# Optimization experiments

Hardware: AMD Instinct MI355X
Metric: run time of the kernel (lower is better)

Reference implementation:

```python
import jax, jax.numpy as jnp
import numpy as np

EPS = 1e-5
HEADS = 8  # heads kwarg of TransformerDecoder


def _ln(x, g, b):
    mu = jnp.mean(x, axis=-1, keepdims=True)
    var = jnp.var(x, axis=-1, keepdims=True)
    return (x - mu) * jax.lax.rsqrt(var + EPS) * g + b


def _expert(params, xt, m, scale):
    """One TransformerDecoder expert (BIT-style): per layer, PreNorm2 cross-attn + residual,
    then PreNorm FeedForward + residual. xt: (B,S,D), m: (B,Nt,D)."""
    an_g, an_b, wq, wk, wv, wo, wo_b, fn_g, fn_b, w1, b1, w2, b2 = params
    L = an_g.shape[0]
    B, S, D = xt.shape
    Nt = m.shape[1]
    for l in range(L):
        xn = _ln(xt, an_g[l], an_b[l])
        mn = _ln(m, an_g[l], an_b[l])  # PreNorm2 norms both streams with the same LN
        q = (xn @ wq[l]).reshape(B, S, HEADS, -1)
        k = (mn @ wk[l]).reshape(B, Nt, HEADS, -1)
        v = (mn @ wv[l]).reshape(B, Nt, HEADS, -1)
        attn = jax.nn.softmax(jnp.einsum('bihd,bjhd->bhij', q, k) * scale, axis=-1)
        o = jnp.einsum('bhij,bjhd->bihd', attn, v).reshape(B, S, -1)
        xt = xt + o @ wo[l] + wo_b[l]
        h = _ln(xt, fn_g[l], fn_b[l])
        xt = xt + jax.nn.gelu(h @ w1[l] + b1[l], approximate=False) @ w2[l] + b2[l]
    return xt


def setup_inputs():
    key = jax.random.key(0)
    ks = iter(jax.random.split(key, 40))
    B, C, H, W = 4, 128, 64, 64
    D, INNER, FF, P, L, NT = 256, 512, 1024, 4, 2, 8
    r = lambda shape, s=1.0: jax.random.normal(next(ks), shape, jnp.float32) * s
    return {
        'x': r((B, C, H, W)),
        'm': r((B, NT, D)),
        'proj_w': r((C, D), 0.05), 'proj_b': r((D,), 0.02),
        'lnp_g': jnp.ones((D,), jnp.float32), 'lnp_b': jnp.zeros((D,), jnp.float32),
        'sq_w': r((D, D), 0.05), 'sq_b': r((D,), 0.02),
        'sk_w': r((D, D), 0.05), 'sk_b': r((D,), 0.02),
        'sv_w': r((D, 1), 0.05), 'sv_b': r((1,), 0.02),
        'an_g': jnp.ones((P, L, D), jnp.float32), 'an_b': jnp.zeros((P, L, D), jnp.float32),
        'wq': r((P, L, D, INNER), 0.05), 'wk': r((P, L, D, INNER), 0.05), 'wv': r((P, L, D, INNER), 0.05),
        'wo': r((P, L, INNER, D), 0.05), 'wo_b': r((P, L, D), 0.02),
        'fn_g': jnp.ones((P, L, D), jnp.float32), 'fn_b': jnp.zeros((P, L, D), jnp.float32),
        'w1': r((P, L, D, FF), 0.05), 'b1': r((P, L, FF), 0.02),
        'w2': r((P, L, FF, D), 0.05), 'b2': r((P, L, D), 0.02),
        'fln_g': jnp.ones((D,), jnp.float32), 'fln_b': jnp.zeros((D,), jnp.float32),
    }


def reference(x, m, proj_w, proj_b, lnp_g, lnp_b, sq_w, sq_b, sk_w, sk_b, sv_w, sv_b,
              an_g, an_b, wq, wk, wv, wo, wo_b, fn_g, fn_b, w1, b1, w2, b2, fln_g, fln_b):
    B, C, H, W = x.shape
    D = proj_w.shape[1]
    # 1x1 conv -> flatten(2).transpose(1,2): row-major (h,w) tokens
    tokens = jnp.einsum('bchw,cd->bhwd', x, proj_w).reshape(B, H * W, D) + proj_b
    tokens = _ln(tokens, lnp_g, lnp_b)
    # TokenScorer: cross-attention importance scores, v projects to scalar
    q = tokens @ sq_w + sq_b
    k = m @ sk_w + sk_b
    v = m @ sv_w + sv_b  # (B, Nt, 1)
    aw = jax.nn.softmax(jnp.einsum('bnd,bmd->bnm', q, k) / jnp.sqrt(jnp.float32(D)), axis=-1)
    scores = jnp.einsum('bnm,bmo->bno', aw, v)[..., 0]  # (B, N)
    P = an_g.shape[0]
    N = tokens.shape[1]
    S = N // P
    # descending sort of token scores
    idx = jnp.argsort(-scores, axis=1)  # (B, N)
    pscores = jnp.take_along_axis(scores, idx, axis=1).reshape(B, P, S).mean(-1)  # (B, P)
    pw = jax.nn.softmax(pscores, axis=1)  # (B, P)
    # gather tokens per partition: (P, B, S, D)
    gathered = jnp.take_along_axis(tokens, idx[..., None], axis=1).reshape(B, P, S, D).transpose(1, 0, 2, 3)
    scale = 1.0 / jnp.sqrt(jnp.float32(D))  # Cross_Attention scale = dim ** -0.5
    params = (an_g, an_b, wq, wk, wv, wo, wo_b, fn_g, fn_b, w1, b1, w2, b2)
    proc = jax.vmap(lambda pr, xt: _expert(pr, xt, m, scale))(params, gathered)  # (P, B, S, D)
    proc = proc * pw.T[:, :, None, None]
    flat = proc.transpose(1, 0, 2, 3).reshape(B, N, D)
    # scatter back into original token order (idx is a permutation)
    out = jnp.zeros_like(tokens).at[jnp.arange(B)[:, None], idx].set(flat)
    return _ln(out, fln_g, fln_b)
```

## Files before the change

kernel.cpp:

```cpp
#include <hip/hip_runtime.h>
#include <hip/hip_bf16.h>
#include <math.h>

#define BB 4
#define CC 128
#define NN 4096
#define DD 256
#define INNER 512
#define FFD 1024
#define PP 4
#define LL 2
#define NT 8
#define SS 1024
#define SCALE 0.0625f

typedef __attribute__((ext_vector_type(8))) short bf16x8;
typedef __attribute__((ext_vector_type(8))) short short8;
typedef __attribute__((ext_vector_type(4))) short short4v;
typedef __attribute__((ext_vector_type(4))) float f32x4;

#define GLD_LDS16(g, l) __builtin_amdgcn_global_load_lds( \
    (const __attribute__((address_space(1))) void*)(g), \
    (__attribute__((address_space(3))) void*)(l), 16, 0, 0)

template<int NW>
__device__ inline float block_sum(float v, float* sbuf){
  #pragma unroll
  for (int mk=32; mk; mk>>=1) v += __shfl_xor(v, mk);
  int w = threadIdx.x>>6;
  if ((threadIdx.x&63)==0) sbuf[w]=v;
  __syncthreads();
  float r = 0.f;
  #pragma unroll
  for (int k=0;k<NW;k++) r += sbuf[k];
  __syncthreads();
  return r;
}

__device__ inline unsigned short bf16bits(float v){
  __hip_bfloat16 t = __float2bfloat16(v);
  unsigned short u;
  __builtin_memcpy(&u, &t, 2);
  return u;
}
__device__ inline float bf2f(unsigned short u){
  unsigned int x = ((unsigned int)u)<<16;
  float f;
  __builtin_memcpy(&f, &x, 4);
  return f;
}

__device__ inline float gelu_f(float x){
  float z  = x * 0.70710678118654752440f;
  float az = fabsf(z);
  float t  = 1.0f / (1.0f + 0.3275911f*az);
  float y  = t*(0.254829592f + t*(-0.284496736f + t*(1.421413741f +
             t*(-1.453152027f + t*1.061405429f))));
  float erfv = 1.0f - y*__expf(-az*az);
  erfv = (z < 0.0f) ? -erfv : erfv;
  return 0.5f*x*(1.0f+erfv);
}

__global__ __launch_bounds__(256) void scorer_kernel(
    const float* __restrict__ m, const float* __restrict__ sk_w,
    const float* __restrict__ sk_b, const float* __restrict__ sv_w,
    const float* __restrict__ sv_b, const float* __restrict__ sq_w,
    const float* __restrict__ sq_b,
    float* __restrict__ kk2, float* __restrict__ kb, float* __restrict__ vsc)
{
  __shared__ float ms[256];
  __shared__ float ks[256];
  __shared__ float sbuf[4];
  int bj = blockIdx.x;
  int tid = threadIdx.x;
  ms[tid] = m[bj*DD + tid];
  __syncthreads();
  float acc=0.f;
  #pragma unroll 8
  for(int c=0;c<DD;c++) acc = fmaf(ms[c], sk_w[c*DD + tid], acc);
  ks[tid] = acc + sk_b[tid];
  float sv = block_sum<4>(ms[tid]*sv_w[tid], sbuf);
  if(tid==0) vsc[bj] = sv + sv_b[0];
  __syncthreads();
  const float* wr = sq_w + (long)tid*DD;
  float a2 = 0.f;
  #pragma unroll 4
  for (int c=0; c<DD; c+=4){
    float4 wvv = *(const float4*)(wr + c);
    a2 = fmaf(wvv.x, ks[c+0], fmaf(wvv.y, ks[c+1], fmaf(wvv.z, ks[c+2], fmaf(wvv.w, ks[c+3], a2))));
  }
  kk2[bj*DD + tid] = a2;
  float kbv = block_sum<4>(sq_b[tid]*ks[tid], sbuf);
  if (tid==0) kb[bj] = kbv;
}

__global__ __launch_bounds__(256) void proj_prep_kernel(
    const float* __restrict__ x, const float* __restrict__ proj_w,
    const float* __restrict__ proj_b, const float* __restrict__ lnp_g,
    const float* __restrict__ lnp_b, const float* __restrict__ kk2,
    const float* __restrict__ kb, const float* __restrict__ vsc,
    float* __restrict__ tokens, float* __restrict__ scores,
    int* __restrict__ rank, long long* __restrict__ psumsI,
    const float* __restrict__ m, const float* __restrict__ an_g,
    const float* __restrict__ an_b, const float* __restrict__ wk,
    const float* __restrict__ wv, float* __restrict__ kvk,
    float* __restrict__ kvv,
    const float* __restrict__ wq, const float* __restrict__ w1,
    const float* __restrict__ w2,
    __hip_bfloat16* __restrict__ wqT, __hip_bfloat16* __restrict__ w1T,
    __hip_bfloat16* __restrict__ w2T)
{
  __shared__ union {
    struct {
      float xs[16][132];
      float ys[16][260];
      float kj[8][260];
      float kbs[8], vs[8], mu_s[16], rs_s[16];
      float lg[16][8];
    } pr;
    struct { float t[64][65]; } wc;
    struct { float mn[256]; float sbuf[4]; } kv;
  } sm;
  int z = blockIdx.x;
  int tid = threadIdx.x;

  if (z < 1024){
    int b  = z >> 8;
    int n0 = (z & 255) * 16;
    if (tid < 16) rank[b*NN + n0 + tid] = 0;
    if (z == 0 && tid < 16) psumsI[tid] = 0;
    float (*xs)[132] = sm.pr.xs;
    float (*ys)[260] = sm.pr.ys;
    float (*kj)[260] = sm.pr.kj;
    float* kbs = sm.pr.kbs; float* vs = sm.pr.vs;
    float* mu_s = sm.pr.mu_s; float* rs_s = sm.pr.rs_s;
    float (*lg)[8] = sm.pr.lg;
    #pragma unroll
    for (int i=0;i<8;i++){
      int l = tid + i*256;
      int t = l & 15, c = l >> 4;
      xs[t][c] = x[(long)(b*CC + c)*NN + n0 + t];
    }
    #pragma unroll
    for (int i=0;i<8;i++){
      int idx = i*256 + tid;
      int r = idx >> 8, c = idx & 255;
      kj[r][c] = kk2[(b*NT + r)*DD + c];
    }
    if (tid < 8){ kbs[tid] = kb[b*NT+tid]; vs[tid] = vsc[b*NT+tid]; }
    __syncthreads();
    float acc[16];
    #pragma unroll
    for (int t=0;t<16;t++) acc[t]=0.f;
    for (int c0=0;c0<CC;c0+=4){
      float w0 = proj_w[(c0+0)*DD + tid];
      float w1_ = proj_w[(c0+1)*DD + tid];
      float w2_ = proj_w[(c0+2)*DD + tid];
      float w3_ = proj_w[(c0+3)*DD + tid];
      #pragma unroll
      for (int t=0;t<16;t++){
        float4 xv = *(const float4*)&xs[t][c0];
        acc[t] = fmaf(xv.x,w0,fmaf(xv.y,w1_,fmaf(xv.z,w2_,fmaf(xv.w,w3_,acc[t]))));
      }
    }
    float pb = proj_b[tid];
    #pragma unroll
    for (int t=0;t<16;t++) ys[t][tid] = acc[t] + pb;
    __syncthreads();
    int w = tid>>6, lane = tid&63;
    for (int k=0;k<4;k++){
      int t = w*4+k;
      float s = ys[t][lane] + ys[t][lane+64] + ys[t][lane+128] + ys[t][lane+192];
      #pragma unroll
      for (int mk=32; mk; mk>>=1) s += __shfl_xor(s, mk);
      float mu = s*(1.0f/256.0f);
      float d0=ys[t][lane]-mu, d1=ys[t][lane+64]-mu, d2=ys[t][lane+128]-mu, d3=ys[t][lane+192]-mu;
      float q = d0*d0+d1*d1+d2*d2+d3*d3;
      #pragma unroll
      for (int mk=32; mk; mk>>=1) q += __shfl_xor(q, mk);
      if (lane==0){ mu_s[t]=mu; rs_s[t]=rsqrtf(q*(1.0f/256.0f)+1e-5f); }
    }
    __syncthreads();
    float g = lnp_g[tid], be = lnp_b[tid];
    #pragma unroll
    for (int t=0;t<16;t++){
      float nv = (ys[t][tid]-mu_s[t])*rs_s[t]*g + be;
      tokens[((long)(b*NN + n0 + t))*DD + tid] = nv;
      ys[t][tid] = nv;
    }
    __syncthreads();
    if (tid < 128){
      int t = tid>>3, j = tid&7;
      float a2 = 0.f;
      for (int c0=0;c0<DD;c0+=4){
        float4 tv = *(const float4*)&ys[t][c0];
        float4 kv2 = *(const float4*)&kj[j][c0];
        a2 = fmaf(tv.x,kv2.x,fmaf(tv.y,kv2.y,fmaf(tv.z,kv2.z,fmaf(tv.w,kv2.w,a2))));
      }
      lg[t][j] = (a2 + kbs[j]) * SCALE;
    }
    __syncthreads();
    if (tid < 16){
      float mx=-1e30f;
      #pragma unroll
      for(int j=0;j<NT;j++) mx=fmaxf(mx,lg[tid][j]);
      float s=0.f, sc=0.f;
      #pragma unroll
      for(int j=0;j<NT;j++){ float e=__expf(lg[tid][j]-mx); s+=e; sc+=e*vs[j]; }
      scores[b*NN + n0 + tid] = sc/s;
    }
  } else if (z < 1280){
    float* mn = sm.kv.mn;
    float* sbuf = sm.kv.sbuf;
    int idx = z - 1024;
    int j = idx & 7, b = (idx>>3)&3, pl = idx>>5;
    float v = m[(b*NT+j)*DD + tid];
    float s = block_sum<4>(v, sbuf);
    float mu = s*(1.0f/256.0f);
    float dv = v-mu;
    float q = block_sum<4>(dv*dv, sbuf);
    float rs = rsqrtf(q*(1.0f/256.0f)+1e-5f);
    mn[tid] = dv*rs*an_g[pl*DD+tid] + an_b[pl*DD+tid];
    __syncthreads();
    float ka0=0.f, va0=0.f, ka1=0.f, va1=0.f;
    const float* wkb = wk + (long)pl*DD*INNER;
    const float* wvb = wv + (long)pl*DD*INNER;
    #pragma unroll 8
    for (int c=0;c<DD;c++){
      float mc = mn[c];
      const float* wkr = wkb + (long)c*INNER;
      const float* wvr = wvb + (long)c*INNER;
      ka0 = fmaf(mc, wkr[tid], ka0);
      ka1 = fmaf(mc, wkr[tid+256], ka1);
      va0 = fmaf(mc, wvr[tid], va0);
      va1 = fmaf(mc, wvr[tid+256], va1);
    }
    long off = ((long)pl*BB + b)*(NT*INNER) + j*INNER;
    kvk[off+tid]=ka0; kvk[off+tid+256]=ka1;
    kvv[off+tid]=va0; kvv[off+tid+256]=va1;
  } else {
    int z2 = z - 1280;
    const float* src; __hip_bfloat16* dst; int K, N, rel;
    if (z2 < 256)      { src=wq; dst=wqT; K=DD;   N=INNER; rel=z2; }
    else if (z2 < 768) { src=w1; dst=w1T; K=DD;   N=FFD;   rel=z2-256; }
    else               { src=w2; dst=w2T; K=FFD;  N=DD;    rel=z2-768; }
    int tn = N>>6, tk = K>>6, per = tn*tk;
    int pl = rel/per, r2 = rel%per;
    int n0 = (r2%tn)*64, k0 = (r2/tn)*64;
    float (*t)[65] = sm.wc.t;
    #pragma unroll
    for (int i=0;i<4;i++){
      int idx = i*256+tid;
      int kk = idx>>4, n4 = idx&15;
      float4 v = *(const float4*)&src[((long)pl*K + k0+kk)*N + n0 + n4*4];
      t[kk][n4*4+0]=v.x; t[kk][n4*4+1]=v.y; t[kk][n4*4+2]=v.z; t[kk][n4*4+3]=v.w;
    }
    __syncthreads();
    #pragma unroll
    for (int i=0;i<4;i++){
      int idx = i*256+tid;
      int nn = idx>>4, k4 = idx&15;
      short4v o;
      o[0] = (short)bf16bits(t[k4*4+0][nn]);
      o[1] = (short)bf16bits(t[k4*4+1][nn]);
      o[2] = (short)bf16bits(t[k4*4+2][nn]);
      o[3] = (short)bf16bits(t[k4*4+3][nn]);
      *(short4v*)&dst[((long)pl*N + n0+nn)*K + k0 + k4*4] = o;
    }
  }
}

__global__ __launch_bounds__(256) void rank_qkvwo_kernel(
    const float* __restrict__ scores, int* __restrict__ rank,
    const float* __restrict__ kvk, const float* __restrict__ kvv,
    const __hip_bfloat16* __restrict__ wqT, const float* __restrict__ wo,
    __hip_bfloat16* __restrict__ qkBuf, __hip_bfloat16* __restrict__ vwoT)
{
  __shared__ union {
    struct { float ss[256]; } rk;
    struct { float kL[8][64]; float vL[8][64]; } qv;
  } sm;
  int z = blockIdx.x;
  if (z < 1024){
    int b  = z >> 8;
    int it = (z >> 4) & 15;
    int jt = z & 15;
    int i = it*256 + threadIdx.x;
    float si = scores[b*NN + i];
    sm.rk.ss[threadIdx.x] = scores[b*NN + jt*256 + threadIdx.x];
    __syncthreads();
    int jbase = jt*256;
    int cnt = 0;
    #pragma unroll 4
    for (int j=0;j<256;j++){
      float sj = sm.rk.ss[j];
      cnt += (sj > si) || (sj == si && (jbase+j) < i);
    }
    atomicAdd(&rank[b*NN+i], cnt);
  } else {
    int zz = z - 1024;
    int z3 = zz>>3, h = zz&7;
    int l = z3>>4, g = z3&15;
    int b = g>>2, p = g&3;
    int pl = p*LL + l;
    int c = threadIdx.x;
    float (*kL)[64] = sm.qv.kL;
    float (*vL)[64] = sm.qv.vL;
    {
      int j0 = c>>6, d0 = c&63;
      long off = ((long)pl*BB + b)*(NT*INNER) + h*64 + d0;
      kL[j0][d0]   = kvk[off + j0*INNER];
      vL[j0][d0]   = kvv[off + j0*INNER];
      kL[j0+4][d0] = kvk[off + (j0+4)*INNER];
      vL[j0+4][d0] = kvv[off + (j0+4)*INNER];
    }
    __syncthreads();
    float qa[8] = {0,0,0,0,0,0,0,0};
    float va[8] = {0,0,0,0,0,0,0,0};
    const __hip_bfloat16* wqp = wqT + ((long)pl*INNER + h*64)*DD + c;
    const float* wop = wo + ((long)pl*INNER + h*64)*DD + c;
    #pragma unroll 4
    for (int d=0; d<64; d++){
      float wqv = bf2f(*(const unsigned short*)(wqp + (long)d*DD));
      float wov = wop[(long)d*DD];
      #pragma unroll
      for (int j=0;j<8;j++){
        qa[j] = fmaf(kL[j][d], wqv, qa[j]);
        va[j] = fmaf(vL[j][d], wov, va[j]);
      }
    }
    __hip_bfloat16* qkg = qkBuf + (long)z3*64*256;
    __hip_bfloat16* vwg = vwoT + (long)z3*256*64;
    #pragma unroll
    for (int j=0;j<8;j++)
      qkg[(h*8+j)*256 + c] = __float2bfloat16(qa[j]*SCALE);
    short8 o;
    #pragma unroll
    for (int j=0;j<8;j++) o[j] = (short)bf16bits(va[j]);
    *(short8*)(vwg + c*64 + h*8) = o;
  }
}

__global__ __launch_bounds__(256) void rank_finalize_kernel(
    const int* __restrict__ rank, const float* __restrict__ scores,
    int* __restrict__ cidx, long long* __restrict__ psumsI)
{
  __shared__ unsigned long long bins[PP];
  if (threadIdx.x < PP) bins[threadIdx.x] = 0ull;
  __syncthreads();
  int b = blockIdx.x >> 4;
  int i = (blockIdx.x & 15)*256 + threadIdx.x;
  int rk = rank[b*NN + i];
  int p = rk >> 10;
  cidx[(b*PP + p)*SS + (rk & (SS-1))] = i;
  long long iv = (long long)llrintf(scores[b*NN + i] * 268435456.0f);
  atomicAdd(&bins[p], (unsigned long long)iv);
  __syncthreads();
  if (threadIdx.x < PP)
    atomicAdd((unsigned long long*)&psumsI[b*PP + threadIdx.x], bins[threadIdx.x]);
}

__global__ __launch_bounds__(256) void gather_ln_kernel(
    const float* __restrict__ tokens, const int* __restrict__ cidx,
    float* __restrict__ Xc, __hip_bfloat16* __restrict__ Y,
    const float* __restrict__ gamma, const float* __restrict__ beta)
{
  long slot = (long)blockIdx.x*8 + (threadIdx.x>>5);
  int l32 = threadIdx.x & 31;
  int b = (int)(slot >> 12);
  int p = (int)((slot>>10)&3);
  int i = cidx[slot];
  const float* src = tokens + ((long)b*NN + i)*DD + l32*8;
  float4 v0 = *(const float4*)src;
  float4 v1 = *(const float4*)(src+4);
  *(float4*)(Xc + slot*DD + l32*8) = v0;
  *(float4*)(Xc + slot*DD + l32*8 + 4) = v1;
  float s = v0.x+v0.y+v0.z+v0.w+v1.x+v1.y+v1.z+v1.w;
  #pragma unroll
  for (int mk=16; mk; mk>>=1) s += __shfl_xor(s, mk);
  float mu = s*(1.0f/256.0f);
  float vv[8] = {v0.x,v0.y,v0.z,v0.w,v1.x,v1.y,v1.z,v1.w};
  float q = 0.f;
  #pragma unroll
  for (int k=0;k<8;k++){ float d = vv[k]-mu; q += d*d; }
  #pragma unroll
  for (int mk=16; mk; mk>>=1) q += __shfl_xor(q, mk);
  float rs = rsqrtf(q*(1.0f/256.0f)+1e-5f);
  short8 o;
  #pragma unroll
  for (int k=0;k<8;k++){
    int d = l32*8+k;
    o[k] = (short)bf16bits((vv[k]-mu)*rs*gamma[p*(LL*DD)+d]+beta[p*(LL*DD)+d]);
  }
  *(short8*)(Y + slot*DD + l32*8) = o;
}

template<bool HASBIAS, bool GELU, bool ACCUM>
__global__ __launch_bounds__(256) void mfma_gemm(
    const __hip_bfloat16* __restrict__ A, long astride, int K,
    const __hip_bfloat16* __restrict__ BT, long bpstride,
    const float* __restrict__ bias, int bias_pstride,
    void* __restrict__ Cp, int ldc, long cstride)
{
  int g = blockIdx.z;
  int p = g & 3;
  const __hip_bfloat16* Ag = A  + (long)g*astride + (long)blockIdx.x*128*K;
  const __hip_bfloat16* Bg = BT + (long)p*bpstride + (long)blockIdx.y*128*K;
  const float* biasg = HASBIAS ? (bias + (long)p*bias_pstride) : nullptr;

  __shared__ __align__(16) __hip_bfloat16 Asm[2][128*64];
  __shared__ __align__(16) __hip_bfloat16 Bsm[2][128*64];

  int tid = threadIdx.x;
  int w = tid>>6, lane = tid&63;
  int wr = w>>1, wc = w&1;
  int lr = lane>>4, lc = lane&15;
  int ldsbase = tid & ~63;

  const __hip_bfloat16* aseg[4];
  const __hip_bfloat16* bseg[4];
  #pragma unroll
  for (int i=0;i<4;i++){
    int seg = i*256 + tid;
    int r = seg>>3, sl = seg&7;
    int sg = sl ^ (r&7);
    aseg[i] = Ag + (long)r*K + sg*8;
    bseg[i] = Bg + (long)r*K + sg*8;
  }

  f32x4 acc[4][4] = {};
  int nt = K >> 6;

  #define STAGE(buf) do { \
    _Pragma("unroll") \
    for (int i_=0;i_<4;i_++) \
      GLD_LDS16(aseg[i_], &Asm[buf][(i_*256 + ldsbase)*8]); \
    _Pragma("unroll") \
    for (int i_=0;i_<4;i_++) \
      GLD_LDS16(bseg[i_], &Bsm[buf][(i_*256 + ldsbase)*8]); \
    _Pragma("unroll") \
    for (int i_=0;i_<4;i_++){ aseg[i_] += 64; bseg[i_] += 64; } \
  } while(0)

  STAGE(0);
  asm volatile("s_waitcnt vmcnt(0)" ::: "memory");
  __syncthreads();

  for (int t=0; t<nt; t++){
    int cur = t & 1;
    if (t+1 < nt) STAGE(cur^1);
    #pragma unroll
    for (int kc=0;kc<2;kc++){
      bf16x8 af[4], bfr[4];
      #pragma unroll
      for (int mi=0;mi<4;mi++){
        int r = wr*64 + mi*16 + lc;
        int s = kc*4 + lr;
        af[mi] = *(const bf16x8*)(&Asm[cur][r*64 + (s ^ (r&7))*8]);
      }
      #pragma unroll
      for (int ni=0;ni<4;ni++){
        int r = wc*64 + ni*16 + lc;
        int s = kc*4 + lr;
        bfr[ni] = *(const bf16x8*)(&Bsm[cur][r*64 + (s ^ (r&7))*8]);
      }
      #pragma unroll
      for (int mi=0;mi<4;mi++)
        #pragma unroll
        for (int ni=0;ni<4;ni++)
          acc[mi][ni] = __builtin_amdgcn_mfma_f32_16x16x32_bf16(af[mi], bfr[ni], acc[mi][ni], 0, 0, 0);
    }
    if (t+1 < nt) asm volatile("s_waitcnt vmcnt(0)" ::: "memory");
    __syncthreads();
  }
  #undef STAGE

  if (ACCUM){
    float* Cg = (float*)Cp + (long)g*cstride;
    #pragma unroll
    for (int ni=0;ni<4;ni++){
      int col = blockIdx.y*128 + wc*64 + ni*16 + lc;
      float bv = HASBIAS ? biasg[col] : 0.0f;
      #pragma unroll
      for (int mi=0;mi<4;mi++){
        int row = blockIdx.x*128 + wr*64 + mi*16 + lr*4;
        #pragma unroll
        for (int j=0;j<4;j++){
          float v = acc[mi][ni][j] + bv;
          if (GELU) v = gelu_f(v);
          Cg[(long)(row+j)*ldc + col] += v;
        }
      }
    }
  } else {
    __hip_bfloat16* Cg = (__hip_bfloat16*)Cp + (long)g*cstride;
    #pragma unroll
    for (int ni=0;ni<4;ni++){
      int col = blockIdx.y*128 + wc*64 + ni*16 + lc;
      float bv = HASBIAS ? biasg[col] : 0.0f;
      #pragma unroll
      for (int mi=0;mi<4;mi++){
        int row = blockIdx.x*128 + wr*64 + mi*16 + lr*4;
        #pragma unroll
        for (int j=0;j<4;j++){
          float v = acc[mi][ni][j] + bv;
          if (GELU) v = gelu_f(v);
          Cg[(long)(row+j)*ldc + col] = __float2bfloat16(v);
        }
      }
    }
  }
}

template<bool LAST>
__global__ __launch_bounds__(256) void ff2_fused_kernel(
    const __hip_bfloat16* __restrict__ F,
    const __hip_bfloat16* __restrict__ w2l,
    const float* __restrict__ b2l,
    float* __restrict__ Xc,
    const float* __restrict__ g_ln,
    const float* __restrict__ b_ln,
    __hip_bfloat16* __restrict__ actOut,
    const int* __restrict__ cidx,
    const long long* __restrict__ psumsI,
    float* __restrict__ out)
{
  int rb = blockIdx.x;
  int g  = blockIdx.y;
  int p  = g & 3;
  const __hip_bfloat16* Ag = F + ((long)g*SS + rb*64)*FFD;
  const __hip_bfloat16* Bg = w2l + (long)p*((long)LL*DD*FFD);

  __shared__ __align__(16) __hip_bfloat16 As[2][64*64];
  __shared__ __align__(16) __hip_bfloat16 Bs[2][256*64];

  int tid = threadIdx.x;
  int w = tid>>6, lane = tid&63;
  int lr = lane>>4, lc = lane&15;
  int ldsbase = tid & ~63;

  const __hip_bfloat16* aseg[2];
  const __hip_bfloat16* bseg[8];
  #pragma unroll
  for (int i=0;i<2;i++){
    int seg = i*256 + tid;
    int r = seg>>3, sl = seg&7;
    aseg[i] = Ag + (long)r*FFD + (sl ^ (r&7))*8;
  }
  #pragma unroll
  for (int i=0;i<8;i++){
    int seg = i*256 + tid;
    int r = seg>>3, sl = seg&7;
    bseg[i] = Bg + (long)r*FFD + (sl ^ (r&7))*8;
  }

  f32x4 acc[4][4] = {};

  #define STAGE2(buf) do { \
    _Pragma("unroll") \
    for (int i_=0;i_<2;i_++) \
      GLD_LDS16(aseg[i_], &As[buf][(i_*256 + ldsbase)*8]); \
    _Pragma("unroll") \
    for (int i_=0;i_<8;i_++) \
      GLD_LDS16(bseg[i_], &Bs[buf][(i_*256 + ldsbase)*8]); \
    _Pragma("unroll") \
    for (int i_=0;i_<2;i_++) aseg[i_] += 64; \
    _Pragma("unroll") \
    for (int i_=0;i_<8;i_++) bseg[i_] += 64; \
  } while(0)

  STAGE2(0);
  asm volatile("s_waitcnt vmcnt(0)" ::: "memory");
  __syncthreads();

  for (int t=0; t<16; t++){
    int cur = t & 1;
    if (t+1 < 16) STAGE2(cur^1);
    #pragma unroll
    for (int kc=0;kc<2;kc++){
      bf16x8 af[4], bfr[4];
      #pragma unroll
      for (int mi=0;mi<4;mi++){
        int r = mi*16 + lc;
        int s = kc*4 + lr;
        af[mi] = *(const bf16x8*)(&As[cur][r*64 + (s ^ (r&7))*8]);
      }
      #pragma unroll
      for (int ni=0;ni<4;ni++){
        int c = w*64 + ni*16 + lc;
        int s = kc*4 + lr;
        bfr[ni] = *(const bf16x8*)(&Bs[cur][c*64 + (s ^ (c&7))*8]);
      }
      #pragma unroll
      for (int mi=0;mi<4;mi++)
        #pragma unroll
        for (int ni=0;ni<4;ni++)
          acc[mi][ni] = __builtin_amdgcn_mfma_f32_16x16x32_bf16(af[mi], bfr[ni], acc[mi][ni], 0, 0, 0);
    }
    if (t+1 < 16) asm volatile("s_waitcnt vmcnt(0)" ::: "memory");
    __syncthreads();
  }
  #undef STAGE2

  __syncthreads();
  float* pfl = (float*)&As[0][0];
  float* pfq = (float*)&As[0][0] + 256;
  float* Xg = Xc + (long)g*SS*DD + (long)rb*64*DD;

  float pwv = 1.0f;
  if (LAST){
    int b = g>>2;
    float ps[4];
    #pragma unroll
    for (int p2=0;p2<4;p2++)
      ps[p2] = (float)((double)psumsI[b*PP+p2] * (1.0/268435456.0/1024.0));
    float mxp = fmaxf(fmaxf(ps[0],ps[1]),fmaxf(ps[2],ps[3]));
    float e0=__expf(ps[0]-mxp), e1=__expf(ps[1]-mxp), e2=__expf(ps[2]-mxp), e3=__expf(ps[3]-mxp);
    float es = e0+e1+e2+e3;
    float ev = (p==0)?e0:(p==1)?e1:(p==2)?e2:e3;
    pwv = ev/es;
  }

  float srow[4][4], qrow[4][4];
  #pragma unroll
  for (int mi=0;mi<4;mi++)
    #pragma unroll
    for (int j=0;j<4;j++){ srow[mi][j]=0.f; qrow[mi][j]=0.f; }
  #pragma unroll
  for (int ni=0;ni<4;ni++){
    int col = w*64 + ni*16 + lc;
    float bv = b2l[p*(LL*DD) + col];
    #pragma unroll
    for (int mi=0;mi<4;mi++){
      int row = mi*16 + lr*4;
      #pragma unroll
      for (int j=0;j<4;j++){
        float v = Xg[(long)(row+j)*DD + col] + acc[mi][ni][j] + bv;
        if (!LAST) Xg[(long)(row+j)*DD + col] = v;
        if (LAST) v *= pwv;
        acc[mi][ni][j] = v;
        srow[mi][j] += v;
        qrow[mi][j] += v*v;
      }
    }
  }
  #pragma unroll
  for (int mi=0;mi<4;mi++)
    #pragma unroll
    for (int j=0;j<4;j++){
      float s2=srow[mi][j], q2=qrow[mi][j];
      s2 += __shfl_xor(s2,1); q2 += __shfl_xor(q2,1);
      s2 += __shfl_xor(s2,2); q2 += __shfl_xor(q2,2);
      s2 += __shfl_xor(s2,4); q2 += __shfl_xor(q2,4);
      s2 += __shfl_xor(s2,8); q2 += __shfl_xor(q2,8);
      srow[mi][j]=s2; qrow[mi][j]=q2;
    }
  if (lc==0){
    #pragma unroll
    for (int mi=0;mi<4;mi++)
      #pragma unroll
      for (int j=0;j<4;j++){
        int row = mi*16 + lr*4 + j;
        pfl[w*64+row] = srow[mi][j];
        pfq[w*64+row] = qrow[mi][j];
      }
  }
  __syncthreads();

  if (!LAST){
    __hip_bfloat16* Ya = actOut + ((long)g*SS + rb*64)*DD;
    const float* fg = g_ln + p*(LL*DD);
    const float* fb = b_ln + p*(LL*DD);
    #pragma unroll
    for (int mi=0;mi<4;mi++){
      #pragma unroll
      for (int j=0;j<4;j++){
        int row = mi*16 + lr*4 + j;
        float S = pfl[row] + pfl[64+row] + pfl[128+row] + pfl[192+row];
        float Q = pfq[row] + pfq[64+row] + pfq[128+row] + pfq[192+row];
        float mu = S*(1.0f/256.0f);
        float var = Q*(1.0f/256.0f) - mu*mu;
        float rs2 = rsqrtf(var + 1e-5f);
        #pragma unroll
        for (int ni=0;ni<4;ni++){
          int col = w*64 + ni*16 + lc;
          Ya[(long)row*DD + col] =
              __float2bfloat16((acc[mi][ni][j]-mu)*rs2*fg[col]+fb[col]);
        }
      }
    }
  } else {
    int b = g>>2;
    #pragma unroll
    for (int mi=0;mi<4;mi++){
      #pragma unroll
      for (int j=0;j<4;j++){
        int row = mi*16 + lr*4 + j;
        long slot = (long)g*SS + rb*64 + row;
        int i = cidx[slot];
        float S = pfl[row] + pfl[64+row] + pfl[128+row] + pfl[192+row];
        float Q = pfq[row] + pfq[64+row] + pfq[128+row] + pfq[192+row];
        float mu = S*(1.0f/256.0f);
        float var = Q*(1.0f/256.0f) - mu*mu;
        float rs2 = rsqrtf(var + 1e-5f);
        float* op = out + ((long)b*NN + i)*DD;
        #pragma unroll
        for (int ni=0;ni<4;ni++){
          int col = w*64 + ni*16 + lc;
          op[col] = (acc[mi][ni][j]-mu)*rs2*g_ln[col]+b_ln[col];
        }
      }
    }
  }
}

__global__ __launch_bounds__(256) void fused_attn_kernel(
    const __hip_bfloat16* __restrict__ actA,
    const __hip_bfloat16* __restrict__ qk,
    const __hip_bfloat16* __restrict__ vwo,
    const float* __restrict__ wo_bl,
    const float* __restrict__ fn_gl,
    const float* __restrict__ fn_bl,
    float* __restrict__ Xc,
    __hip_bfloat16* __restrict__ actOut)
{
  int rb = blockIdx.x;
  int g  = blockIdx.y;
  int p  = g & 3;
  const __hip_bfloat16* Ag = actA + ((long)g*SS + rb*64)*DD;
  const __hip_bfloat16* Qg = qk  + (long)g*64*256;
  const __hip_bfloat16* Vg = vwo + (long)g*256*64;

  __shared__ __align__(16) __hip_bfloat16 sm[24576];
  int tid = threadIdx.x;
  int w = tid>>6, lane = tid&63;
  int lr = lane>>4, lc = lane&15;
  int ldsbase = tid & ~63;

  #pragma unroll
  for (int i=0;i<8;i++){
    int seg = i*256 + tid;
    int r = seg>>5, sl = seg&31;
    int sg = sl ^ (r&7);
    GLD_LDS16(Qg + (long)r*256 + sg*8, &sm[8192 + (i*256 + ldsbase)*8]);
  }
  #pragma unroll
  for (int i=0;i<2;i++){
    int seg = i*256 + tid;
    int r = seg>>3, sl = seg&7;
    int sg = sl ^ (r&7);
    GLD_LDS16(Ag + (long)r*DD + sg*8, &sm[0 + (i*256 + ldsbase)*8]);
  }
  asm volatile("s_waitcnt vmcnt(0)" ::: "memory");
  __syncthreads();

  f32x4 acc1[4] = {};
  for (int t=0; t<4; t++){
    int cur = t&1;
    if (t+1 < 4){
      #pragma unroll
      for (int i=0;i<2;i++){
        int seg = i*256 + tid;
        int r = seg>>3, sl = seg&7;
        int sg = sl ^ (r&7);
        GLD_LDS16(Ag + (long)r*DD + (t+1)*64 + sg*8,
                  &sm[(cur^1)*4096 + (i*256 + ldsbase)*8]);
      }
    }
    #pragma unroll
    for (int kc=0;kc<2;kc++){
      int r = w*16 + lc;
      int s = kc*4 + lr;
      bf16x8 af = *(const bf16x8*)(&sm[cur*4096 + r*64 + (s ^ (r&7))*8]);
      #pragma unroll
      for (int ni=0;ni<4;ni++){
        int rb_ = ni*16 + lc;
        int sb = t*8 + kc*4 + lr;
        bf16x8 bfr = *(const bf16x8*)(&sm[8192 + rb_*256 + (sb ^ (rb_&7))*8]);
        acc1[ni] = __builtin_amdgcn_mfma_f32_16x16x32_bf16(af, bfr, acc1[ni], 0, 0, 0);
      }
    }
    if (t+1 < 4) asm volatile("s_waitcnt vmcnt(0)" ::: "memory");
    __syncthreads();
  }

  #pragma unroll
  for (int i=0;i<8;i++){
    int seg = i*256 + tid;
    int r = seg>>3, sl = seg&7;
    int sg = sl ^ (r&7);
    GLD_LDS16(Vg + (long)r*64 + sg*8, &sm[8192 + (i*256 + ldsbase)*8]);
  }

  float pv[4][4];
  #pragma unroll
  for (int ni=0;ni<4;ni++){
    #pragma unroll
    for (int j=0;j<4;j++){
      float v = acc1[ni][j];
      float mx = v;
      mx = fmaxf(mx, __shfl_xor(mx,1));
      mx = fmaxf(mx, __shfl_xor(mx,2));
      mx = fmaxf(mx, __shfl_xor(mx,4));
      float e = __expf(v - mx);
      float ssum = e;
      ssum += __shfl_xor(ssum,1);
      ssum += __shfl_xor(ssum,2);
      ssum += __shfl_xor(ssum,4);
      pv[ni][j] = e / ssum;
    }
  }
  #pragma unroll
  for (int ni=0;ni<4;ni++){
    #pragma unroll
    for (int j=0;j<4;j++){
      int row = w*16 + lr*4 + j;
      int col = ni*16 + lc;
      int s = col>>3, e = col&7;
      sm[row*64 + ((s ^ (row&7))<<3) + e] = __float2bfloat16(pv[ni][j]);
    }
  }
  asm volatile("s_waitcnt vmcnt(0)" ::: "memory");
  __syncthreads();

  f32x4 acc2[4][4] = {};
  #pragma unroll
  for (int kc=0;kc<2;kc++){
    bf16x8 af[4], bfr[4];
    #pragma unroll
    for (int mi=0;mi<4;mi++){
      int r = mi*16 + lc;
      int s = kc*4 + lr;
      af[mi] = *(const bf16x8*)(&sm[r*64 + (s ^ (r&7))*8]);
    }
    #pragma unroll
    for (int ni=0;ni<4;ni++){
      int rb_ = w*64 + ni*16 + lc;
      int s = kc*4 + lr;
      bfr[ni] = *(const bf16x8*)(&sm[8192 + rb_*64 + (s ^ (rb_&7))*8]);
    }
    #pragma unroll
    for (int mi=0;mi<4;mi++)
      #pragma unroll
      for (int ni=0;ni<4;ni++)
        acc2[mi][ni] = __builtin_amdgcn_mfma_f32_16x16x32_bf16(af[mi], bfr[ni], acc2[mi][ni], 0, 0, 0);
  }

  __syncthreads();
  float* pfl = (float*)sm;
  float* pfq = (float*)sm + 256;
  float* Xg = Xc + (long)g*SS*DD + (long)rb*64*DD;
  float srow[4][4], qrow[4][4];
  #pragma unroll
  for (int mi=0;mi<4;mi++)
    #pragma unroll
    for (int j=0;j<4;j++){ srow[mi][j]=0.f; qrow[mi][j]=0.f; }
  #pragma unroll
  for (int ni=0;ni<4;ni++){
    int col = w*64 + ni*16 + lc;
    float bv = wo_bl[p*(LL*DD) + col];
    #pragma unroll
    for (int mi=0;mi<4;mi++){
      int row = mi*16 + lr*4;
      #pragma unroll
      for (int j=0;j<4;j++){
        float v = Xg[(long)(row+j)*DD + col] + acc2[mi][ni][j] + bv;
        Xg[(long)(row+j)*DD + col] = v;
        acc2[mi][ni][j] = v;
        srow[mi][j] += v;
        qrow[mi][j] += v*v;
      }
    }
  }
  #pragma unroll
  for (int mi=0;mi<4;mi++)
    #pragma unroll
    for (int j=0;j<4;j++){
      float s2=srow[mi][j], q2=qrow[mi][j];
      s2 += __shfl_xor(s2,1); q2 += __shfl_xor(q2,1);
      s2 += __shfl_xor(s2,2); q2 += __shfl_xor(q2,2);
      s2 += __shfl_xor(s2,4); q2 += __shfl_xor(q2,4);
      s2 += __shfl_xor(s2,8); q2 += __shfl_xor(q2,8);
      srow[mi][j]=s2; qrow[mi][j]=q2;
    }
  if (lc==0){
    #pragma unroll
    for (int mi=0;mi<4;mi++)
      #pragma unroll
      for (int j=0;j<4;j++){
        int row = mi*16 + lr*4 + j;
        pfl[w*64+row] = srow[mi][j];
        pfq[w*64+row] = qrow[mi][j];
      }
  }
  __syncthreads();
  __hip_bfloat16* Ya = actOut + ((long)g*SS + rb*64)*DD;
  const float* fg = fn_gl + p*(LL*DD);
  const float* fb = fn_bl + p*(LL*DD);
  #pragma unroll
  for (int mi=0;mi<4;mi++){
    #pragma unroll
    for (int j=0;j<4;j++){
      int row = mi*16 + lr*4 + j;
      float S = pfl[row] + pfl[64+row] + pfl[128+row] + pfl[192+row];
      float Q = pfq[row] + pfq[64+row] + pfq[128+row] + pfq[192+row];
      float mu = S*(1.0f/256.0f);
      float var = Q*(1.0f/256.0f) - mu*mu;
      float rs2 = rsqrtf(var + 1e-5f);
      #pragma unroll
      for (int ni=0;ni<4;ni++){
        int col = w*64 + ni*16 + lc;
        Ya[(long)row*DD + col] =
            __float2bfloat16((acc2[mi][ni][j]-mu)*rs2*fg[col]+fb[col]);
      }
    }
  }
}

extern "C" void kernel_launch(void* const* d_in, const int* in_sizes, int n_in,
                              void* d_out, int out_size, void* d_ws, size_t ws_size,
                              hipStream_t stream)
{
  (void)in_sizes; (void)n_in; (void)out_size; (void)ws_size;
  const float* x     =(const float*)d_in[0];
  const float* m     =(const float*)d_in[1];
  const float* proj_w=(const float*)d_in[2];
  const float* proj_b=(const float*)d_in[3];
  const float* lnp_g =(const float*)d_in[4];
  const float* lnp_b =(const float*)d_in[5];
  const float* sq_w  =(const float*)d_in[6];
  const float* sq_b  =(const float*)d_in[7];
  const float* sk_w  =(const float*)d_in[8];
  const float* sk_b  =(const float*)d_in[9];
  const float* sv_w  =(const float*)d_in[10];
  const float* sv_b  =(const float*)d_in[11];
  const float* an_g  =(const float*)d_in[12];
  const float* an_b  =(const float*)d_in[13];
  const float* wq    =(const float*)d_in[14];
  const float* wk    =(const float*)d_in[15];
  const float* wv    =(const float*)d_in[16];
  const float* wo    =(const float*)d_in[17];
  const float* wo_b  =(const float*)d_in[18];
  const float* fn_g  =(const float*)d_in[19];
  const float* fn_b  =(const float*)d_in[20];
  const float* w1    =(const float*)d_in[21];
  const float* b1    =(const float*)d_in[22];
  const float* w2    =(const float*)d_in[23];
  const float* b2    =(const float*)d_in[24];
  const float* fln_g =(const float*)d_in[25];
  const float* fln_b =(const float*)d_in[26];
  float* out = (float*)d_out;

  float* ws = (float*)d_ws;
  float* tokens  = ws;  ws += 4194304;
  ws += 4194304;
  float* Xc      = ws;  ws += 4194304;
  float* actAf   = ws;  ws += 2097152;
  float* wqTf    = ws;  ws += 524288;
  float* w1Tf    = ws;  ws += 1048576;
  float* w2Tf    = ws;  ws += 1048576;
  float* qkBf    = ws;  ws += 262144;
  float* vwoTf   = ws;  ws += 262144;
  float* kvk     = ws;  ws += 131072;
  float* kvv     = ws;  ws += 131072;
  float* kk2     = ws;  ws += 8192;
  float* kb      = ws;  ws += 32;
  float* vsc     = ws;  ws += 64;
  float* scores  = ws;  ws += 16384;
  long long* psumsI = (long long*)ws;  ws += 32;
  int* rank      = (int*)ws;  ws += 16384;
  int* cidx      = (int*)ws;  ws += 16384;

  __hip_bfloat16* actA  = (__hip_bfloat16*)actAf;
  __hip_bfloat16* actF  = (__hip_bfloat16*)tokens;
  __hip_bfloat16* wqT   = (__hip_bfloat16*)wqTf;
  __hip_bfloat16* w1T   = (__hip_bfloat16*)w1Tf;
  __hip_bfloat16* w2T   = (__hip_bfloat16*)w2Tf;
  __hip_bfloat16* qkBuf = (__hip_bfloat16*)qkBf;
  __hip_bfloat16* vwoT  = (__hip_bfloat16*)vwoTf;

  scorer_kernel<<<32,256,0,stream>>>(m, sk_w, sk_b, sv_w, sv_b, sq_w, sq_b,
                                     kk2, kb, vsc);
  proj_prep_kernel<<<2560,256,0,stream>>>(
      x, proj_w, proj_b, lnp_g, lnp_b, kk2, kb, vsc,
      tokens, scores, rank, psumsI,
      m, an_g, an_b, wk, wv, kvk, kvv,
      wq, w1, w2, wqT, w1T, w2T);
  rank_qkvwo_kernel<<<1280,256,0,stream>>>(scores, rank, kvk, kvv, wqT, wo,
                                           qkBuf, vwoT);
  rank_finalize_kernel<<<64,256,0,stream>>>(rank, scores, cidx, psumsI);
  gather_ln_kernel<<<2048,256,0,stream>>>(tokens, cidx, Xc, actA, an_g, an_b);

  fused_attn_kernel<<<dim3(16,16),256,0,stream>>>(
      actA, qkBuf, vwoT, wo_b, fn_g, fn_b, Xc, actA);
  mfma_gemm<true,true,false><<<dim3(8,8,16),256,0,stream>>>(
      actA, (long)SS*DD, DD, w1T, (long)LL*FFD*DD,
      b1, LL*FFD, actF, FFD, (long)SS*FFD);
  ff2_fused_kernel<false><<<dim3(16,16),256,0,stream>>>(
      actF, w2T, b2, Xc, an_g + DD, an_b + DD, actA,
      nullptr, nullptr, nullptr);
  fused_attn_kernel<<<dim3(16,16),256,0,stream>>>(
      actA, qkBuf + (long)16*64*256, vwoT + (long)16*256*64,
      wo_b + DD, fn_g + DD, fn_b + DD, Xc, actA);
  mfma_gemm<true,true,false><<<dim3(8,8,16),256,0,stream>>>(
      actA, (long)SS*DD, DD, w1T + (long)FFD*DD, (long)LL*FFD*DD,
      b1 + FFD, LL*FFD, actF, FFD, (long)SS*FFD);
  ff2_fused_kernel<true><<<dim3(16,16),256,0,stream>>>(
      actF, w2T + (long)DD*FFD, b2 + DD, Xc, fln_g, fln_b, nullptr,
      cidx, psumsI, out);
}
```

Measured before the change: 244.7 us.

## Defer layer-2 weight conversion into FF1 GEMM, fuse rank finalize with gather-LN

Result: slower. 266.3 us (+8.8%).

```diff
diff --git a/kernel.cpp b/kernel.cpp
--- a/kernel.cpp
+++ b/kernel.cpp
@@ -59,6 +59,32 @@
   float erfv = 1.0f - y*__expf(-az*az);
   erfv = (z < 0.0f) ? -erfv : erfv;
   return 0.5f*x*(1.0f+erfv);
+}
+
+__device__ inline void wconv_tile(const float* __restrict__ src,
+                                  __hip_bfloat16* __restrict__ dst,
+                                  int pl, int K, int N, int k0, int n0,
+                                  float (*t)[65], int tid)
+{
+  #pragma unroll
+  for (int i=0;i<4;i++){
+    int idx = i*256+tid;
+    int kk = idx>>4, n4 = idx&15;
+    float4 v = *(const float4*)&src[((long)pl*K + k0+kk)*N + n0 + n4*4];
+    t[kk][n4*4+0]=v.x; t[kk][n4*4+1]=v.y; t[kk][n4*4+2]=v.z; t[kk][n4*4+3]=v.w;
+  }
+  __syncthreads();
+  #pragma unroll
+  for (int i=0;i<4;i++){
+    int idx = i*256+tid;
+    int nn = idx>>4, k4 = idx&15;
+    short4v o;
+    o[0] = (short)bf16bits(t[k4*4+0][nn]);
+    o[1] = (short)bf16bits(t[k4*4+1][nn]);
+    o[2] = (short)bf16bits(t[k4*4+2][nn]);
+    o[3] = (short)bf16bits(t[k4*4+3][nn]);
+    *(short4v*)&dst[((long)pl*N + n0+nn)*K + k0 + k4*4] = o;
+  }
 }
 
 __global__ __launch_bounds__(256) void scorer_kernel(
@@ -209,10 +235,11 @@
       for(int j=0;j<NT;j++){ float e=__expf(lg[tid][j]-mx); s+=e; sc+=e*vs[j]; }
       scores[b*NN + n0 + tid] = sc/s;
     }
-  } else if (z < 1280){
+  } else if (z < 1536){
     float* mn = sm.kv.mn;
     float* sbuf = sm.kv.sbuf;
-    int idx = z - 1024;
+    int idx2 = z - 1024;
+    int idx = idx2>>1, half = idx2&1;
     int j = idx & 7, b = (idx>>3)&3, pl = idx>>5;
     float v = m[(b*NT+j)*DD + tid];
     float s = block_sum<4>(v, sbuf);
@@ -222,50 +249,31 @@
     float rs = rsqrtf(q*(1.0f/256.0f)+1e-5f);
     mn[tid] = dv*rs*an_g[pl*DD+tid] + an_b[pl*DD+tid];
     __syncthreads();
-    float ka0=0.f, va0=0.f, ka1=0.f, va1=0.f;
-    const float* wkb = wk + (long)pl*DD*INNER;
-    const float* wvb = wv + (long)pl*DD*INNER;
+    float ka=0.f, va=0.f;
+    int col = half*256 + tid;
+    const float* wkb = wk + (long)pl*DD*INNER + col;
+    const float* wvb = wv + (long)pl*DD*INNER + col;
     #pragma unroll 8
     for (int c=0;c<DD;c++){
       float mc = mn[c];
-      const float* wkr = wkb + (long)c*INNER;
-      const float* wvr = wvb + (long)c*INNER;
-      ka0 = fmaf(mc, wkr[tid], ka0);
-      ka1 = fmaf(mc, wkr[tid+256], ka1);
-      va0 = fmaf(mc, wvr[tid], va0);
-      va1 = fmaf(mc, wvr[tid+256], va1);
-    }
-    long off = ((long)pl*BB + b)*(NT*INNER) + j*INNER;
-    kvk[off+tid]=ka0; kvk[off+tid+256]=ka1;
-    kvv[off+tid]=va0; kvv[off+tid+256]=va1;
+      ka = fmaf(mc, wkb[(long)c*INNER], ka);
+      va = fmaf(mc, wvb[(long)c*INNER], va);
+    }
+    long off = ((long)pl*BB + b)*(NT*INNER) + j*INNER + col;
+    kvk[off]=ka; kvv[off]=va;
   } else {
-    int z2 = z - 1280;
-    const float* src; __hip_bfloat16* dst; int K, N, rel;
-    if (z2 < 256)      { src=wq; dst=wqT; K=DD;   N=INNER; rel=z2; }
-    else if (z2 < 768) { src=w1; dst=w1T; K=DD;   N=FFD;   rel=z2-256; }
-    else               { src=w2; dst=w2T; K=FFD;  N=DD;    rel=z2-768; }
-    int tn = N>>6, tk = K>>6, per = tn*tk;
-    int pl = rel/per, r2 = rel%per;
-    int n0 = (r2%tn)*64, k0 = (r2/tn)*64;
-    float (*t)[65] = sm.wc.t;
-    #pragma unroll
-    for (int i=0;i<4;i++){
-      int idx = i*256+tid;
-      int kk = idx>>4, n4 = idx&15;
-      float4 v = *(const float4*)&src[((long)pl*K + k0+kk)*N + n0 + n4*4];
-      t[kk][n4*4+0]=v.x; t[kk][n4*4+1]=v.y; t[kk][n4*4+2]=v.z; t[kk][n4*4+3]=v.w;
-    }
-    __syncthreads();
-    #pragma unroll
-    for (int i=0;i<4;i++){
-      int idx = i*256+tid;
-      int nn = idx>>4, k4 = idx&15;
-      short4v o;
-      o[0] = (short)bf16bits(t[k4*4+0][nn]);
-      o[1] = (short)bf16bits(t[k4*4+1][nn]);
-      o[2] = (short)bf16bits(t[k4*4+2][nn]);
-      o[3] = (short)bf16bits(t[k4*4+3][nn]);
-      *(short4v*)&dst[((long)pl*N + n0+nn)*K + k0 + k4*4] = o;
+    int z2 = z - 1536;
+    if (z2 < 256){
+      int pl = z2/32, r2 = z2%32;
+      wconv_tile(wq, wqT, pl, DD, INNER, (r2/8)*64, (r2%8)*64, sm.wc.t, tid);
+    } else if (z2 < 512){
+      int rel = z2-256;
+      int p = rel/64, r2 = rel%64;
+      wconv_tile(w1, w1T, p*2, DD, FFD, (r2/16)*64, (r2%16)*64, sm.wc.t, tid);
+    } else {
+      int rel = z2-512;
+      int p = rel/64, r2 = rel%64;
+      wconv_tile(w2, w2T, p*2, FFD, DD, (r2/4)*64, (r2%4)*64, sm.wc.t, tid);
     }
   }
 }
@@ -341,35 +349,28 @@
   }
 }
 
-__global__ __launch_bounds__(256) void rank_finalize_kernel(
-    const int* __restrict__ rank, const float* __restrict__ scores,
-    int* __restrict__ cidx, long long* __restrict__ psumsI)
+__global__ __launch_bounds__(256) void scatter_ln_kernel(
+    const float* __restrict__ tokens, const int* __restrict__ rank,
+    const float* __restrict__ scores,
+    int* __restrict__ cidx, long long* __restrict__ psumsI,
+    float* __restrict__ Xc, __hip_bfloat16* __restrict__ Y,
+    const float* __restrict__ gamma, const float* __restrict__ beta)
 {
   __shared__ unsigned long long bins[PP];
   if (threadIdx.x < PP) bins[threadIdx.x] = 0ull;
   __syncthreads();
-  int b = blockIdx.x >> 4;
-  int i = (blockIdx.x & 15)*256 + threadIdx.x;
+  long row = (long)blockIdx.x*8 + (threadIdx.x>>5);
+  int l32 = threadIdx.x & 31;
+  int b = (int)(row >> 12);
+  int i = (int)(row & 4095);
   int rk = rank[b*NN + i];
   int p = rk >> 10;
-  cidx[(b*PP + p)*SS + (rk & (SS-1))] = i;
-  long long iv = (long long)llrintf(scores[b*NN + i] * 268435456.0f);
-  atomicAdd(&bins[p], (unsigned long long)iv);
-  __syncthreads();
-  if (threadIdx.x < PP)
-    atomicAdd((unsigned long long*)&psumsI[b*PP + threadIdx.x], bins[threadIdx.x]);
-}
-
-__global__ __launch_bounds__(256) void gather_ln_kernel(
-    const float* __restrict__ tokens, const int* __restrict__ cidx,
-    float* __restrict__ Xc, __hip_bfloat16* __restrict__ Y,
-    const float* __restrict__ gamma, const float* __restrict__ beta)
-{
-  long slot = (long)blockIdx.x*8 + (threadIdx.x>>5);
-  int l32 = threadIdx.x & 31;
-  int b = (int)(slot >> 12);
-  int p = (int)((slot>>10)&3);
-  int i = cidx[slot];
+  long slot = (long)(b*PP + p)*SS + (rk & (SS-1));
+  if (l32 == 0){
+    cidx[slot] = i;
+    long long iv = (long long)llrintf(scores[b*NN + i] * 268435456.0f);
+    atomicAdd(&bins[p], (unsigned long long)iv);
+  }
   const float* src = tokens + ((long)b*NN + i)*DD + l32*8;
   float4 v0 = *(const float4*)src;
   float4 v1 = *(const float4*)(src+4);
@@ -393,6 +394,9 @@
     o[k] = (short)bf16bits((vv[k]-mu)*rs*gamma[p*(LL*DD)+d]+beta[p*(LL*DD)+d]);
   }
   *(short8*)(Y + slot*DD + l32*8) = o;
+  __syncthreads();
+  if (threadIdx.x < PP)
+    atomicAdd((unsigned long long*)&psumsI[b*PP + threadIdx.x], bins[threadIdx.x]);
 }
 
 template<bool HASBIAS, bool GELU, bool ACCUM>
@@ -400,18 +404,40 @@
     const __hip_bfloat16* __restrict__ A, long astride, int K,
     const __hip_bfloat16* __restrict__ BT, long bpstride,
     const float* __restrict__ bias, int bias_pstride,
-    void* __restrict__ Cp, int ldc, long cstride)
+    void* __restrict__ Cp, int ldc, long cstride,
+    const float* __restrict__ w1src, const float* __restrict__ w2src,
+    __hip_bfloat16* __restrict__ w1dst, __hip_bfloat16* __restrict__ w2dst)
 {
-  int g = blockIdx.z;
+  __shared__ union {
+    struct {
+      __hip_bfloat16 Asm[2][128*64];
+      __hip_bfloat16 Bsm[2][128*64];
+    } g;
+    struct { float t[64][65]; } wc;
+  } smu;
+  int gid = blockIdx.x;
+  int tid = threadIdx.x;
+  if (gid >= 1024){
+    int z2 = gid - 1024;
+    if (z2 < 256){
+      int p = z2/64, r2 = z2%64;
+      wconv_tile(w1src, w1dst, p*2+1, DD, FFD, (r2/16)*64, (r2%16)*64, smu.wc.t, tid);
+    } else {
+      int rel = z2-256;
+      int p = rel/64, r2 = rel%64;
+      wconv_tile(w2src, w2dst, p*2+1, FFD, DD, (r2/4)*64, (r2%4)*64, smu.wc.t, tid);
+    }
+    return;
+  }
+  int bx = gid & 7, by = (gid>>3)&7, g = gid>>6;
   int p = g & 3;
-  const __hip_bfloat16* Ag = A  + (long)g*astride + (long)blockIdx.x*128*K;
-  const __hip_bfloat16* Bg = BT + (long)p*bpstride + (long)blockIdx.y*128*K;
+  const __hip_bfloat16* Ag = A  + (long)g*astride + (long)bx*128*K;
+  const __hip_bfloat16* Bg = BT + (long)p*bpstride + (long)by*128*K;
   const float* biasg = HASBIAS ? (bias + (long)p*bias_pstride) : nullptr;
 
-  __shared__ __align__(16) __hip_bfloat16 Asm[2][128*64];
-  __shared__ __align__(16) __hip_bfloat16 Bsm[2][128*64];
-
-  int tid = threadIdx.x;
+  __hip_bfloat16 (*Asm)[128*64] = smu.g.Asm;
+  __hip_bfloat16 (*Bsm)[128*64] = smu.g.Bsm;
+
   int w = tid>>6, lane = tid&63;
   int wr = w>>1, wc = w&1;
   int lr = lane>>4, lc = lane&15;
@@ -479,11 +505,11 @@
     float* Cg = (float*)Cp + (long)g*cstride;
     #pragma unroll
     for (int ni=0;ni<4;ni++){
-      int col = blockIdx.y*128 + wc*64 + ni*16 + lc;
+      int col = by*128 + wc*64 + ni*16 + lc;
       float bv = HASBIAS ? biasg[col] : 0.0f;
       #pragma unroll
       for (int mi=0;mi<4;mi++){
-        int row = blockIdx.x*128 + wr*64 + mi*16 + lr*4;
+        int row = bx*128 + wr*64 + mi*16 + lr*4;
         #pragma unroll
         for (int j=0;j<4;j++){
           float v = acc[mi][ni][j] + bv;
@@ -496,11 +522,11 @@
     __hip_bfloat16* Cg = (__hip_bfloat16*)Cp + (long)g*cstride;
     #pragma unroll
     for (int ni=0;ni<4;ni++){
-      int col = blockIdx.y*128 + wc*64 + ni*16 + lc;
+      int col = by*128 + wc*64 + ni*16 + lc;
       float bv = HASBIAS ? biasg[col] : 0.0f;
       #pragma unroll
       for (int mi=0;mi<4;mi++){
-        int row = blockIdx.x*128 + wr*64 + mi*16 + lr*4;
+        int row = bx*128 + wr*64 + mi*16 + lr*4;
         #pragma unroll
         for (int j=0;j<4;j++){
           float v = acc[mi][ni][j] + bv;
@@ -981,30 +1007,32 @@
 
   scorer_kernel<<<32,256,0,stream>>>(m, sk_w, sk_b, sv_w, sv_b, sq_w, sq_b,
                                      kk2, kb, vsc);
-  proj_prep_kernel<<<2560,256,0,stream>>>(
+  proj_prep_kernel<<<2304,256,0,stream>>>(
       x, proj_w, proj_b, lnp_g, lnp_b, kk2, kb, vsc,
       tokens, scores, rank, psumsI,
       m, an_g, an_b, wk, wv, kvk, kvv,
       wq, w1, w2, wqT, w1T, w2T);
   rank_qkvwo_kernel<<<1280,256,0,stream>>>(scores, rank, kvk, kvv, wqT, wo,
                                            qkBuf, vwoT);
-  rank_finalize_kernel<<<64,256,0,stream>>>(rank, scores, cidx, psumsI);
-  gather_ln_kernel<<<2048,256,0,stream>>>(tokens, cidx, Xc, actA, an_g, an_b);
+  scatter_ln_kernel<<<2048,256,0,stream>>>(tokens, rank, scores, cidx, psumsI,
+                                           Xc, actA, an_g, an_b);
 
   fused_attn_kernel<<<dim3(16,16),256,0,stream>>>(
       actA, qkBuf, vwoT, wo_b, fn_g, fn_b, Xc, actA);
-  mfma_gemm<true,true,false><<<dim3(8,8,16),256,0,stream>>>(
+  mfma_gemm<true,true,false><<<1536,256,0,stream>>>(
       actA, (long)SS*DD, DD, w1T, (long)LL*FFD*DD,
-      b1, LL*FFD, actF, FFD, (long)SS*FFD);
+      b1, LL*FFD, actF, FFD, (long)SS*FFD,
+      w1, w2, w1T, w2T);
   ff2_fused_kernel<false><<<dim3(16,16),256,0,stream>>>(
       actF, w2T, b2, Xc, an_g + DD, an_b + DD, actA,
       nullptr, nullptr, nullptr);
   fused_attn_kernel<<<dim3(16,16),256,0,stream>>>(
       actA, qkBuf + (long)16*64*256, vwoT + (long)16*256*64,
       wo_b + DD, fn_g + DD, fn_b + DD, Xc, actA);
-  mfma_gemm<true,true,false><<<dim3(8,8,16),256,0,stream>>>(
+  mfma_gemm<true,true,false><<<1024,256,0,stream>>>(
       actA, (long)SS*DD, DD, w1T + (long)FFD*DD, (long)LL*FFD*DD,
-      b1 + FFD, LL*FFD, actF, FFD, (long)SS*FFD);
+      b1 + FFD, LL*FFD, actF, FFD, (long)SS*FFD,
+      nullptr, nullptr, nullptr, nullptr);
   ff2_fused_kernel<true><<<dim3(16,16),256,0,stream>>>(
       actF, w2T + (long)DD*FFD, b2 + DD, Xc, fln_g, fln_b, nullptr,
       cidx, psumsI, out);
```
